# Kernel optimization log

Hardware: AMD Instinct MI355X
Metric: run time of the kernel (lower is better)

The kernel has to match this reference:

```python
import jax, jax.numpy as jnp
import numpy as np

K_POOL = 5

def _conv_lookahead(x, W):
    # Faithful to F.conv2d(pad=(fs//2+1,0)) followed by keeping the last L rows:
    # for fs=3 this reduces to out[t] = sum_j x[t+j] @ W[:,j,:].T (2 trailing zeros).
    # x: [..., L, E], W: [nf, fs, E] -> out [..., L, nf]
    fs = W.shape[1]
    L = x.shape[-2]
    pad = [(0, 0)] * (x.ndim - 2) + [(0, fs - 1), (0, 0)]
    xp = jnp.pad(x, pad)
    out = sum(jnp.einsum('...le,fe->...lf', jax.lax.dynamic_slice_in_dim(xp, j, L, axis=-2), W[:, j, :]) for j in range(fs))
    return out

def _cosine(q, s):
    # q: [B,Q,D], s: [B,S,L,D] -> [B,S,Q,L]
    num = jnp.einsum('bqd,bsld->bsql', q, s)
    qn = jnp.linalg.norm(q, axis=-1)  # [B,Q]
    sn = jnp.linalg.norm(s, axis=-1)  # [B,S,L]
    return num / (qn[:, None, :, None] * sn[:, :, None, :])

def _pool(sim, k=K_POOL):
    # sort-based k-max pooling over last dim -> (max, mean-of-top-k), matching torch.sort + slice
    top = jax.lax.top_k(sim, k)[0]            # [..., Q, k] descending
    return jnp.stack([top[..., 0], top.mean(-1)], axis=-1)  # [..., Q, 2]

def _bce(p, t):
    return -(t * jnp.log(p) + (1.0 - t) * jnp.log(1.0 - p)).mean()

def setup_inputs() -> dict:
    key = jax.random.key(0)
    ks = jax.random.split(key, 9)
    B, S, L, Q, V, E, NF, FS = 16, 48, 64, 32, 50000, 300, 256, 3
    return {
        'sentences': jax.random.randint(ks[0], (B, S, L), 0, V, dtype=jnp.int64 if jax.config.jax_enable_x64 else jnp.int32).astype(jnp.int32),
        'question': jax.random.randint(ks[1], (B, Q), 0, V).astype(jnp.int32),
        'target_sents': jax.random.randint(ks[2], (B, S), 0, 2).astype(jnp.int32),
        'target_docs': jax.random.randint(ks[3], (B,), 0, 2).astype(jnp.int32),
        'similarity_one_hot': jax.random.uniform(ks[4], (B, S, Q, L), dtype=jnp.float32),
        'embeds': jax.random.normal(ks[5], (V, E), dtype=jnp.float32),
        'conv_w': jax.random.normal(ks[6], (NF, FS, E), dtype=jnp.float32),
        'lin_w': jax.random.normal(ks[7], (1, 6), dtype=jnp.float32),
        'lin_b': jax.random.normal(ks[8], (1,), dtype=jnp.float32),
    }

def reference(sentences, question, target_sents, target_docs, similarity_one_hot, embeds, conv_w, lin_w, lin_b):
    q_emb = embeds[question]            # [B,Q,E]
    s_emb = embeds[sentences]           # [B,S,L,E]
    q_conv = _conv_lookahead(q_emb, conv_w)   # [B,Q,NF]
    s_conv = _conv_lookahead(s_emb, conv_w)   # [B,S,L,NF]

    sim_ins = _cosine(q_emb, s_emb)     # [B,S,Q,L]
    qmask = (question > 1).astype(sim_ins.dtype)   # [B,Q]
    smask = (sentences > 1).astype(sim_ins.dtype)  # [B,S,L]
    sim_ins = sim_ins * qmask[:, None, :, None] * smask[:, :, None, :]

    sim_sens = _cosine(q_conv, s_conv)  # [B,S,Q,L]

    feats = jnp.concatenate([_pool(sim_ins), _pool(sim_sens), _pool(similarity_one_hot)], axis=-1)  # [B,S,Q,6]
    lo = jax.nn.sigmoid(jnp.einsum('bsqf,of->bsqo', feats, lin_w)[..., 0] + lin_b[0])  # [B,S,Q]
    sent_output = lo.mean(-1)           # [B,S]

    sal = _bce(sent_output, target_sents.astype(sent_output.dtype))
    doc_emit = sent_output.max(-1)      # [B]
    dal = _bce(doc_emit, target_docs.astype(doc_emit.dtype))
    total_loss = (sal + dal) / 2.0
    return (total_loss, sent_output, doc_emit)
```

## Files before the change

kernel.cpp:

```cpp
#include <hip/hip_runtime.h>
#include <math.h>

#define NB 16
#define NS 48
#define NL 64
#define NQ 32
#define NE 300
#define NF 256
#define KP 320
#define QROWS 36

typedef __attribute__((ext_vector_type(8))) short short8;
typedef __attribute__((ext_vector_type(4))) float f32x4;

#define MFMA(a,b,c) __builtin_amdgcn_mfma_f32_16x16x32_bf16((a),(b),(c),0,0,0)

__device__ __forceinline__ unsigned short f2bf(float f) {
    unsigned u = __float_as_uint(f);
    u += 0x7fff + ((u >> 16) & 1);
    return (unsigned short)(u >> 16);
}

#define SE_PITCH 640
#define SC_PITCH 512
#define SIM_OFF (66 * 640)
#define SIM_PITCH 66
#define DYN_LDS (SIM_OFF + NQ * SIM_PITCH * 4)

__device__ __forceinline__ float wave_reduce_sum(float v) {
#pragma unroll
    for (int off = 32; off; off >>= 1) v += __shfl_xor(v, off, 64);
    return v;
}

__device__ __forceinline__ void top5_pool4(float v0, float v1, float v2, float v3,
                                           int lane, float* mx, float* mn) {
    float s0 = 0.f, s1 = 0.f, s2 = 0.f, s3 = 0.f;
    float x0 = 0.f, x1 = 0.f, x2 = 0.f, x3 = 0.f;
#pragma unroll
    for (int i = 0; i < 5; ++i) {
        float m0 = v0, m1 = v1, m2 = v2, m3 = v3;
#pragma unroll
        for (int off = 32; off; off >>= 1) {
            m0 = fmaxf(m0, __shfl_xor(m0, off, 64));
            m1 = fmaxf(m1, __shfl_xor(m1, off, 64));
            m2 = fmaxf(m2, __shfl_xor(m2, off, 64));
            m3 = fmaxf(m3, __shfl_xor(m3, off, 64));
        }
        if (i == 0) { x0 = m0; x1 = m1; x2 = m2; x3 = m3; }
        s0 += m0; s1 += m1; s2 += m2; s3 += m3;
        unsigned long long k0 = __ballot(v0 == m0);
        unsigned long long k1 = __ballot(v1 == m1);
        unsigned long long k2 = __ballot(v2 == m2);
        unsigned long long k3 = __ballot(v3 == m3);
        if (lane == __ffsll(k0) - 1) v0 = -3.4e38f;
        if (lane == __ffsll(k1) - 1) v1 = -3.4e38f;
        if (lane == __ffsll(k2) - 1) v2 = -3.4e38f;
        if (lane == __ffsll(k3) - 1) v3 = -3.4e38f;
    }
    mx[0] = x0; mx[1] = x1; mx[2] = x2; mx[3] = x3;
    mn[0] = s0 * 0.2f; mn[1] = s1 * 0.2f; mn[2] = s2 * 0.2f; mn[3] = s3 * 0.2f;
}

__global__ void wb2_kernel(const float* __restrict__ conv_w, short8* __restrict__ Wb2,
                           unsigned int* __restrict__ done_ctr) {
    if (blockIdx.x == 0 && threadIdx.x == 0) done_ctr[0] = 0u;
    int i = blockIdx.x * 256 + threadIdx.x;
    if (i >= 120 * 256) return;
    int rl = i & 15;
    int ftile = (i >> 4) & 15;
    int c = i >> 8;
    int kg = c & 3, rest = c >> 2;
    int ks = rest % 10, j = rest / 10;
    int f = ftile * 16 + rl;
    int k0 = ks * 32 + kg * 8;
    const float* src = conv_w + (size_t)(f * 3 + j) * NE;
    short8 h;
#pragma unroll
    for (int e = 0; e < 8; ++e) {
        int k = k0 + e;
        h[e] = (short)((k < NE) ? f2bf(src[k]) : (unsigned short)0);
    }
    Wb2[i] = h;
}

__global__ void qe_kernel(const int* __restrict__ question, const float* __restrict__ embeds,
                          unsigned short* __restrict__ qe, short8* __restrict__ qef,
                          float* __restrict__ q_norm) {
    int row = blockIdx.x;
    int b = row / QROWS, r = row % QROWS;
    int l = threadIdx.x;
    unsigned short* dst = qe + (size_t)row * KP;
    if (r < NQ) {
        int tok = question[b * NQ + r];
        const float4* rp = (const float4*)(embeds + (size_t)tok * NE);
        short8 h = {0, 0, 0, 0, 0, 0, 0, 0};
        float ss = 0.f;
        if (l < 38) {
            float4 v0 = rp[2 * l];
            ss += v0.x * v0.x + v0.y * v0.y + v0.z * v0.z + v0.w * v0.w;
            h[0] = (short)f2bf(v0.x); h[1] = (short)f2bf(v0.y);
            h[2] = (short)f2bf(v0.z); h[3] = (short)f2bf(v0.w);
            if (2 * l + 1 < 75) {
                float4 v1 = rp[2 * l + 1];
                ss += v1.x * v1.x + v1.y * v1.y + v1.z * v1.z + v1.w * v1.w;
                h[4] = (short)f2bf(v1.x); h[5] = (short)f2bf(v1.y);
                h[6] = (short)f2bf(v1.z); h[7] = (short)f2bf(v1.w);
            }
        }
        if (l < 40) {
            *(short8*)(dst + 8 * l) = h;
            qef[((size_t)(b * 2 + (r >> 4)) * 40 + l) * 16 + (r & 15)] = h;
        }
        ss = wave_reduce_sum(ss);
        if (l == 0) q_norm[b * NQ + r] = sqrtf(ss);
    } else {
        if (l < 40) {
            short8 z = {0, 0, 0, 0, 0, 0, 0, 0};
            *(short8*)(dst + 8 * l) = z;
        }
    }
}

__global__ __launch_bounds__(256) void qconv_mfma_kernel(
        const unsigned short* __restrict__ qe, const short8* __restrict__ Wb2,
        short8* __restrict__ qcf) {
    __shared__ unsigned short tile[NQ][72];
    int b = blockIdx.x >> 2, fq = blockIdx.x & 3;
    int tid = threadIdx.x, lane = tid & 63, w = tid >> 6;
    int rl = lane & 15, kg = lane >> 4;
    int ftile = fq * 4 + w;
    f32x4 acc0 = (f32x4){0.f, 0.f, 0.f, 0.f};
    f32x4 acc1 = (f32x4){0.f, 0.f, 0.f, 0.f};
    for (int j = 0; j < 3; ++j) {
#pragma unroll 2
        for (int ks = 0; ks < 10; ++ks) {
            int k = ks * 32 + kg * 8;
            int c = (j * 10 + ks) * 4 + kg;
            short8 a0 = *(const short8*)(qe + ((size_t)(b * QROWS) + rl + j) * KP + k);
            short8 a1 = *(const short8*)(qe + ((size_t)(b * QROWS) + 16 + rl + j) * KP + k);
            short8 bb = Wb2[(c * 16 + ftile) * 16 + rl];
            acc0 = MFMA(a0, bb, acc0);
            acc1 = MFMA(a1, bb, acc1);
        }
    }
    int fl = w * 16 + rl;
#pragma unroll
    for (int reg = 0; reg < 4; ++reg) {
        tile[kg * 4 + reg][fl] = f2bf(acc0[reg]);
        tile[16 + kg * 4 + reg][fl] = f2bf(acc1[reg]);
    }
    __syncthreads();
    int mh = tid >> 7, c_local = (tid >> 4) & 7, rl2 = tid & 15;
    short8 h = *(const short8*)(&tile[mh * 16 + rl2][c_local * 8]);
    qcf[((size_t)(b * 2 + mh) * 32 + 8 * fq + c_local) * 16 + rl2] = h;
}

__global__ __launch_bounds__(256) void qcn_kernel(const short8* __restrict__ qcf,
                                                  float* __restrict__ qc_norm) {
    __shared__ float part[2][16][8];
    int b = blockIdx.x;
    int tid = threadIdx.x;
    int mh = tid >> 7, sub = (tid >> 4) & 7, rl = tid & 15;
    const short8* base = qcf + ((size_t)(b * 2 + mh) * 32) * 16;
    float ss = 0.f;
#pragma unroll
    for (int i = 0; i < 4; ++i) {
        short8 h = base[(sub * 4 + i) * 16 + rl];
#pragma unroll
        for (int e = 0; e < 8; ++e) {
            float v = __uint_as_float(((unsigned)(unsigned short)h[e]) << 16);
            ss += v * v;
        }
    }
    part[mh][rl][sub] = ss;
    __syncthreads();
    if (tid < 32) {
        int m2 = tid >> 4, r2 = tid & 15;
        float s = 0.f;
#pragma unroll
        for (int k = 0; k < 8; ++k) s += part[m2][r2][k];
        qc_norm[b * NQ + m2 * 16 + r2] = sqrtf(s);
    }
}

extern __shared__ char ldsc[];
__global__ __launch_bounds__(256, 3) void fused6_kernel(
    const int* __restrict__ sentences, const int* __restrict__ question,
    const float* __restrict__ sim_oh, const float* __restrict__ embeds,
    const short8* __restrict__ Wb2,
    const short8* __restrict__ qef, const short8* __restrict__ qcf,
    const float* __restrict__ q_norm, const float* __restrict__ qc_norm,
    const float* __restrict__ lin_w, const float* __restrict__ lin_b,
    const int* __restrict__ tsent, const int* __restrict__ tdoc,
    unsigned int* __restrict__ done_ctr,
    float* __restrict__ sent_ws, float* __restrict__ d_out)
{
    __shared__ int toks[NL];
    __shared__ float smaskf[NL], snorm[NL], scnorm[NL];
    __shared__ float qn_s[NQ], qcn_s[NQ], qmf_s[NQ];
    __shared__ float wq[4];
    __shared__ float fpool[NQ][2];
    __shared__ int lastflag;
    __shared__ float red2[4];
    __shared__ float dred[NB];

    int tid = threadIdx.x, lane = tid & 63, w = tid >> 6;
    int rl = lane & 15, kg = lane >> 4;
    int bs = blockIdx.x, b = bs / NS;
    int t = (w << 4) + rl, t7 = t & 7;

    if (tid < NL) {
        int tk = sentences[(size_t)bs * NL + tid];
        toks[tid] = tk;
        smaskf[tid] = (tk > 1) ? 1.f : 0.f;
    } else if (tid < NL + NQ) {
        int q = tid - NL;
        qn_s[q] = q_norm[b * NQ + q];
    } else if (tid < NL + 2 * NQ) {
        int q = tid - NL - NQ;
        qcn_s[q] = qc_norm[b * NQ + q];
    } else if (tid < NL + 3 * NQ) {
        int q = tid - NL - 2 * NQ;
        qmf_s[q] = (question[b * NQ + q] > 1) ? 1.f : 0.f;
    }
    __syncthreads();

#pragma unroll 2
    for (int r = w; r < 66; r += 4) {
        char* rowbase = ldsc + r * SE_PITCH;
        int m7 = r & 7;
        if (r < NL) {
            const float4* rp = (const float4*)(embeds + (size_t)toks[r] * NE);
            {
                float4 v = rp[lane];
                ushort4 h = {f2bf(v.x), f2bf(v.y), f2bf(v.z), f2bf(v.w)};
                *(ushort4*)(rowbase + (((lane >> 1) ^ m7) << 4) + ((lane & 1) << 3)) = h;
            }
            if (lane < 11) {
                float4 v = rp[64 + lane];
                ushort4 h = {f2bf(v.x), f2bf(v.y), f2bf(v.z), f2bf(v.w)};
                int g = 64 + lane;
                *(ushort4*)(rowbase + (((g >> 1) ^ m7) << 4) + ((g & 1) << 3)) = h;
            }
            if (lane < 5) {
                int pk = 37 + ((lane + 1) >> 1);
                int sub = ((lane + 1) & 1) << 3;
                *(unsigned long long*)(rowbase + ((pk ^ m7) << 4) + sub) = 0ull;
            }
        } else {
            if (lane < 40) {
                uint4 z = {0, 0, 0, 0};
                *(uint4*)(rowbase + (lane << 4)) = z;
            }
        }
    }
    __syncthreads();

    {
        f32x4 iacc0 = (f32x4){0.f, 0.f, 0.f, 0.f};
        f32x4 iacc1 = (f32x4){0.f, 0.f, 0.f, 0.f};
        f32x4 nB = (f32x4){0.f, 0.f, 0.f, 0.f};
        const short8* qf = qef + (size_t)(b * 80) * 16;
#pragma unroll 2
        for (int ks = 0; ks < 10; ++ks) {
            int c = ks * 4 + kg;
            short8 bB = *(const short8*)(ldsc + t * SE_PITCH + ((c ^ t7) << 4));
            short8 a0 = qf[c * 16 + rl];
            short8 a1 = qf[(40 + c) * 16 + rl];
            iacc0 = MFMA(a0, bB, iacc0);
            iacc1 = MFMA(a1, bB, iacc1);
            nB = MFMA(bB, bB, nB);
        }
        if (kg == (rl >> 2)) snorm[t] = sqrtf(nB[rl & 3]);
        __syncthreads();

        float inv_t = smaskf[t] / snorm[t];
#pragma unroll
        for (int reg = 0; reg < 4; ++reg) {
            int q0 = kg * 4 + reg;
            float s0 = iacc0[reg] / qn_s[q0] * inv_t * qmf_s[q0];
            *(float*)(ldsc + SIM_OFF + (q0 * SIM_PITCH + t) * 4) = s0;
            int q1 = 16 + kg * 4 + reg;
            float s1 = iacc1[reg] / qn_s[q1] * inv_t * qmf_s[q1];
            *(float*)(ldsc + SIM_OFF + (q1 * SIM_PITCH + t) * 4) = s1;
        }
    }
    __syncthreads();

    {
        int q0 = w << 3;
        float v[8];
#pragma unroll
        for (int qi = 0; qi < 8; ++qi)
            v[qi] = *(float*)(ldsc + SIM_OFF + ((q0 + qi) * SIM_PITCH + lane) * 4);
        float mx[4], mn[4];
        top5_pool4(v[0], v[1], v[2], v[3], lane, mx, mn);
        if (lane == 0)
#pragma unroll
            for (int p = 0; p < 4; ++p) { fpool[q0 + p][0] = mx[p]; fpool[q0 + p][1] = mn[p]; }
        top5_pool4(v[4], v[5], v[6], v[7], lane, mx, mn);
        if (lane == 0)
#pragma unroll
            for (int p = 0; p < 4; ++p) { fpool[q0 + 4 + p][0] = mx[p]; fpool[q0 + 4 + p][1] = mn[p]; }
    }

    f32x4 cacc[4][4];
#pragma unroll
    for (int m = 0; m < 4; ++m)
#pragma unroll
        for (int nn = 0; nn < 4; ++nn) cacc[m][nn] = (f32x4){0.f, 0.f, 0.f, 0.f};
    for (int j = 0; j < 3; ++j) {
#pragma unroll 2
        for (int ks = 0; ks < 10; ++ks) {
            int c = (j * 10 + ks) * 4 + kg;
            short8 a[4], bb[4];
#pragma unroll
            for (int m = 0; m < 4; ++m) {
                int row = m * 16 + rl + j;
                a[m] = *(const short8*)(ldsc + row * SE_PITCH +
                                        ((((ks << 2) + kg) ^ (row & 7)) << 4));
            }
#pragma unroll
            for (int nn = 0; nn < 4; ++nn)
                bb[nn] = Wb2[(c * 16 + (w * 4 + nn)) * 16 + rl];
#pragma unroll
            for (int m = 0; m < 4; ++m)
#pragma unroll
                for (int nn = 0; nn < 4; ++nn)
                    cacc[m][nn] = MFMA(a[m], bb[nn], cacc[m][nn]);
        }
    }
    __syncthreads();

#pragma unroll
    for (int m = 0; m < 4; ++m)
#pragma unroll
        for (int nn = 0; nn < 4; ++nn) {
            int f = (w * 4 + nn) * 16 + rl;
#pragma unroll
            for (int reg = 0; reg < 4; ++reg) {
                int tr = m * 16 + kg * 4 + reg;
                *(unsigned short*)(ldsc + tr * SC_PITCH +
                                   (((f >> 3) ^ (tr & 7)) << 4) + ((f & 7) << 1)) =
                    f2bf(cacc[m][nn][reg]);
            }
        }
    __syncthreads();

    float oh[8];
#pragma unroll
    for (int qi = 0; qi < 8; ++qi) {
        int q = (w << 3) + qi;
        oh[qi] = sim_oh[((size_t)bs * NQ + q) * NL + lane];
    }
    {
        f32x4 sacc0 = (f32x4){0.f, 0.f, 0.f, 0.f};
        f32x4 sacc1 = (f32x4){0.f, 0.f, 0.f, 0.f};
        f32x4 nB = (f32x4){0.f, 0.f, 0.f, 0.f};
        const short8* qc = qcf + (size_t)(b * 64) * 16;
#pragma unroll 2
        for (int ks = 0; ks < 8; ++ks) {
            int c = ks * 4 + kg;
            short8 bB = *(const short8*)(ldsc + t * SC_PITCH + ((c ^ t7) << 4));
            short8 a0 = qc[c * 16 + rl];
            short8 a1 = qc[(32 + c) * 16 + rl];
            sacc0 = MFMA(a0, bB, sacc0);
            sacc1 = MFMA(a1, bB, sacc1);
            nB = MFMA(bB, bB, nB);
        }
        if (kg == (rl >> 2)) scnorm[t] = sqrtf(nB[rl & 3]);
        __syncthreads();

        float inv_t = 1.f / scnorm[t];
#pragma unroll
        for (int reg = 0; reg < 4; ++reg) {
            int q0 = kg * 4 + reg;
            *(float*)(ldsc + SIM_OFF + (q0 * SIM_PITCH + t) * 4) =
                sacc0[reg] / qcn_s[q0] * inv_t;
            int q1 = 16 + kg * 4 + reg;
            *(float*)(ldsc + SIM_OFF + (q1 * SIM_PITCH + t) * 4) =
                sacc1[reg] / qcn_s[q1] * inv_t;
        }
    }
    __syncthreads();

    {
        float lw0 = lin_w[0], lw1 = lin_w[1], lw2 = lin_w[2];
        float lw3 = lin_w[3], lw4 = lin_w[4], lw5 = lin_w[5];
        float lb = lin_b[0];
        int q0 = w << 3;
        float sv[8];
#pragma unroll
        for (int qi = 0; qi < 8; ++qi)
            sv[qi] = *(float*)(ldsc + SIM_OFF + ((q0 + qi) * SIM_PITCH + lane) * 4);
        float mxs[8], mns[8], mxo[8], mno[8];
        top5_pool4(sv[0], sv[1], sv[2], sv[3], lane, mxs, mns);
        top5_pool4(sv[4], sv[5], sv[6], sv[7], lane, mxs + 4, mns + 4);
        top5_pool4(oh[0], oh[1], oh[2], oh[3], lane, mxo, mno);
        top5_pool4(oh[4], oh[5], oh[6], oh[7], lane, mxo + 4, mno + 4);
        float psum = 0.f;
#pragma unroll
        for (int qi = 0; qi < 8; ++qi) {
            float f0 = fpool[q0 + qi][0], f1 = fpool[q0 + qi][1];
            float z = f0 * lw0 + f1 * lw1 + mxs[qi] * lw2 + mns[qi] * lw3 +
                      mxo[qi] * lw4 + mno[qi] * lw5 + lb;
            psum += 1.f / (1.f + expf(-z));
        }
        if (lane == 0) wq[w] = psum;
    }
    __syncthreads();
    if (tid == 0) {
        float sent = (wq[0] + wq[1] + wq[2] + wq[3]) * (1.f / 32.f);
        __hip_atomic_store(&sent_ws[bs], sent, __ATOMIC_RELEASE, __HIP_MEMORY_SCOPE_AGENT);
        d_out[1 + bs] = sent;
        unsigned old = atomicAdd(done_ctr, 1u);
        lastflag = (old == (unsigned)(NB * NS - 1)) ? 1 : 0;
    }
    __syncthreads();

    if (lastflag) {
        float acc_l = 0.f;
        for (int i = tid; i < NB * NS; i += 256) {
            float p = __hip_atomic_load(&sent_ws[i], __ATOMIC_ACQUIRE, __HIP_MEMORY_SCOPE_AGENT);
            float tt2 = (float)tsent[i];
            acc_l += tt2 * logf(p) + (1.f - tt2) * logf(1.f - p);
        }
        acc_l = wave_reduce_sum(acc_l);
        if ((tid & 63) == 0) red2[tid >> 6] = acc_l;
        if (tid < NB) {
            float m = -3.4e38f;
            for (int s = 0; s < NS; ++s)
                m = fmaxf(m, __hip_atomic_load(&sent_ws[tid * NS + s], __ATOMIC_ACQUIRE,
                                               __HIP_MEMORY_SCOPE_AGENT));
            d_out[1 + NB * NS + tid] = m;
            float tt2 = (float)tdoc[tid];
            dred[tid] = tt2 * logf(m) + (1.f - tt2) * logf(1.f - m);
        }
        __syncthreads();
        if (tid == 0) {
            float sal = -(red2[0] + red2[1] + red2[2] + red2[3]) / (float)(NB * NS);
            float dsum = 0.f;
            for (int i = 0; i < NB; ++i) dsum += dred[i];
            float dal = -dsum / (float)NB;
            d_out[0] = 0.5f * (sal + dal);
        }
    }
}

extern "C" void kernel_launch(void* const* d_in, const int* in_sizes, int n_in,
                              void* d_out, int out_size, void* d_ws, size_t ws_size,
                              hipStream_t stream) {
    const int* sentences = (const int*)d_in[0];
    const int* question = (const int*)d_in[1];
    const int* tsent = (const int*)d_in[2];
    const int* tdoc = (const int*)d_in[3];
    const float* sim_oh = (const float*)d_in[4];
    const float* embeds = (const float*)d_in[5];
    const float* conv_w = (const float*)d_in[6];
    const float* lin_w = (const float*)d_in[7];
    const float* lin_b = (const float*)d_in[8];
    float* out = (float*)d_out;

    char* wsc = (char*)d_ws;
    short8* Wb2            = (short8*)(wsc);
    unsigned short* qe_old = (unsigned short*)(wsc + 491520);
    short8* qef            = (short8*)(wsc + 860160);
    short8* qcf            = (short8*)(wsc + 1187840);
    float* q_norm          = (float*)(wsc + 1449984);
    float* qc_norm         = (float*)(wsc + 1452032);
    float* sent_ws         = (float*)(wsc + 1454080);
    unsigned int* done_ctr = (unsigned int*)(wsc + 1457152);

    hipFuncSetAttribute(reinterpret_cast<const void*>(fused6_kernel),
                        hipFuncAttributeMaxDynamicSharedMemorySize, DYN_LDS);

    wb2_kernel<<<120, 256, 0, stream>>>(conv_w, Wb2, done_ctr);
    qe_kernel<<<NB * QROWS, 64, 0, stream>>>(question, embeds, qe_old, qef, q_norm);
    qconv_mfma_kernel<<<NB * 4, 256, 0, stream>>>(qe_old, Wb2, qcf);
    qcn_kernel<<<NB, 256, 0, stream>>>(qcf, qc_norm);
    fused6_kernel<<<NB * NS, 256, DYN_LDS, stream>>>(
        sentences, question, sim_oh, embeds, Wb2, qef, qcf, q_norm, qc_norm,
        lin_w, lin_b, tsent, tdoc, done_ctr, sent_ws, out);
}
```

Baseline: 130.6 us.

## Double fused kernel block to 512 threads, splitting work across eight waves

Raises the fused per-sentence kernel from 4 to 8 waves per block. Each wave now handles half the question rows in the cosine MFMAs and half the filter tiles in the conv GEMM, which halves per-wave accumulator registers. The goal is more waves in flight per block to hide the embedding gather and global loads, and less serial work per wave. The cost is redundant B-operand LDS reads across waves (the norm MFMA is kept only on waves 0-3) and larger blocks. Occupancy now depends on LDS size and the new launch bounds.

After: 173.4 us. +32.7%, slower.

```diff
diff --git a/kernel.cpp b/kernel.cpp
--- a/kernel.cpp
+++ b/kernel.cpp
@@ -185,7 +185,7 @@
 }
 
 extern __shared__ char ldsc[];
-__global__ __launch_bounds__(256, 3) void fused6_kernel(
+__global__ __launch_bounds__(512, 4) void fused7_kernel(
     const int* __restrict__ sentences, const int* __restrict__ question,
     const float* __restrict__ sim_oh, const float* __restrict__ embeds,
     const short8* __restrict__ Wb2,
@@ -199,16 +199,17 @@
     __shared__ int toks[NL];
     __shared__ float smaskf[NL], snorm[NL], scnorm[NL];
     __shared__ float qn_s[NQ], qcn_s[NQ], qmf_s[NQ];
-    __shared__ float wq[4];
+    __shared__ float wq[8];
     __shared__ float fpool[NQ][2];
     __shared__ int lastflag;
-    __shared__ float red2[4];
+    __shared__ float red2[8];
     __shared__ float dred[NB];
 
     int tid = threadIdx.x, lane = tid & 63, w = tid >> 6;
     int rl = lane & 15, kg = lane >> 4;
+    int mh = w >> 2, tt = w & 3;
     int bs = blockIdx.x, b = bs / NS;
-    int t = (w << 4) + rl, t7 = t & 7;
+    int t = (tt << 4) + rl, t7 = t & 7;
 
     if (tid < NL) {
         int tk = sentences[(size_t)bs * NL + tid];
@@ -227,7 +228,7 @@
     __syncthreads();
 
 #pragma unroll 2
-    for (int r = w; r < 66; r += 4) {
+    for (int r = w; r < 66; r += 8) {
         char* rowbase = ldsc + r * SE_PITCH;
         int m7 = r & 7;
         if (r < NL) {
@@ -258,63 +259,53 @@
     __syncthreads();
 
     {
-        f32x4 iacc0 = (f32x4){0.f, 0.f, 0.f, 0.f};
-        f32x4 iacc1 = (f32x4){0.f, 0.f, 0.f, 0.f};
+        f32x4 iacc = (f32x4){0.f, 0.f, 0.f, 0.f};
         f32x4 nB = (f32x4){0.f, 0.f, 0.f, 0.f};
-        const short8* qf = qef + (size_t)(b * 80) * 16;
+        const short8* qf = qef + ((size_t)(b * 2 + mh) * 40) * 16;
 #pragma unroll 2
         for (int ks = 0; ks < 10; ++ks) {
             int c = ks * 4 + kg;
             short8 bB = *(const short8*)(ldsc + t * SE_PITCH + ((c ^ t7) << 4));
             short8 a0 = qf[c * 16 + rl];
-            short8 a1 = qf[(40 + c) * 16 + rl];
-            iacc0 = MFMA(a0, bB, iacc0);
-            iacc1 = MFMA(a1, bB, iacc1);
-            nB = MFMA(bB, bB, nB);
-        }
-        if (kg == (rl >> 2)) snorm[t] = sqrtf(nB[rl & 3]);
+            iacc = MFMA(a0, bB, iacc);
+            if (w < 4) nB = MFMA(bB, bB, nB);
+        }
+        if (w < 4 && kg == (rl >> 2)) snorm[t] = sqrtf(nB[rl & 3]);
         __syncthreads();
 
         float inv_t = smaskf[t] / snorm[t];
 #pragma unroll
         for (int reg = 0; reg < 4; ++reg) {
-            int q0 = kg * 4 + reg;
-            float s0 = iacc0[reg] / qn_s[q0] * inv_t * qmf_s[q0];
-            *(float*)(ldsc + SIM_OFF + (q0 * SIM_PITCH + t) * 4) = s0;
-            int q1 = 16 + kg * 4 + reg;
-            float s1 = iacc1[reg] / qn_s[q1] * inv_t * qmf_s[q1];
-            *(float*)(ldsc + SIM_OFF + (q1 * SIM_PITCH + t) * 4) = s1;
+            int q = mh * 16 + kg * 4 + reg;
+            float s0 = iacc[reg] / qn_s[q] * inv_t * qmf_s[q];
+            *(float*)(ldsc + SIM_OFF + (q * SIM_PITCH + t) * 4) = s0;
         }
     }
     __syncthreads();
 
     {
-        int q0 = w << 3;
-        float v[8];
-#pragma unroll
-        for (int qi = 0; qi < 8; ++qi)
-            v[qi] = *(float*)(ldsc + SIM_OFF + ((q0 + qi) * SIM_PITCH + lane) * 4);
+        int q0 = w << 2;
+        float v0 = *(float*)(ldsc + SIM_OFF + ((q0 + 0) * SIM_PITCH + lane) * 4);
+        float v1 = *(float*)(ldsc + SIM_OFF + ((q0 + 1) * SIM_PITCH + lane) * 4);
+        float v2 = *(float*)(ldsc + SIM_OFF + ((q0 + 2) * SIM_PITCH + lane) * 4);
+        float v3 = *(float*)(ldsc + SIM_OFF + ((q0 + 3) * SIM_PITCH + lane) * 4);
         float mx[4], mn[4];
-        top5_pool4(v[0], v[1], v[2], v[3], lane, mx, mn);
+        top5_pool4(v0, v1, v2, v3, lane, mx, mn);
         if (lane == 0)
 #pragma unroll
             for (int p = 0; p < 4; ++p) { fpool[q0 + p][0] = mx[p]; fpool[q0 + p][1] = mn[p]; }
-        top5_pool4(v[4], v[5], v[6], v[7], lane, mx, mn);
-        if (lane == 0)
-#pragma unroll
-            for (int p = 0; p < 4; ++p) { fpool[q0 + 4 + p][0] = mx[p]; fpool[q0 + 4 + p][1] = mn[p]; }
-    }
-
-    f32x4 cacc[4][4];
+    }
+
+    f32x4 cacc[4][2];
 #pragma unroll
     for (int m = 0; m < 4; ++m)
 #pragma unroll
-        for (int nn = 0; nn < 4; ++nn) cacc[m][nn] = (f32x4){0.f, 0.f, 0.f, 0.f};
+        for (int nn = 0; nn < 2; ++nn) cacc[m][nn] = (f32x4){0.f, 0.f, 0.f, 0.f};
     for (int j = 0; j < 3; ++j) {
 #pragma unroll 2
         for (int ks = 0; ks < 10; ++ks) {
             int c = (j * 10 + ks) * 4 + kg;
-            short8 a[4], bb[4];
+            short8 a[4], bb[2];
 #pragma unroll
             for (int m = 0; m < 4; ++m) {
                 int row = m * 16 + rl + j;
@@ -322,12 +313,12 @@
                                         ((((ks << 2) + kg) ^ (row & 7)) << 4));
             }
 #pragma unroll
-            for (int nn = 0; nn < 4; ++nn)
-                bb[nn] = Wb2[(c * 16 + (w * 4 + nn)) * 16 + rl];
+            for (int nn = 0; nn < 2; ++nn)
+                bb[nn] = Wb2[(c * 16 + ((w << 1) + nn)) * 16 + rl];
 #pragma unroll
             for (int m = 0; m < 4; ++m)
 #pragma unroll
-                for (int nn = 0; nn < 4; ++nn)
+                for (int nn = 0; nn < 2; ++nn)
                     cacc[m][nn] = MFMA(a[m], bb[nn], cacc[m][nn]);
         }
     }
@@ -336,8 +327,8 @@
 #pragma unroll
     for (int m = 0; m < 4; ++m)
 #pragma unroll
-        for (int nn = 0; nn < 4; ++nn) {
-            int f = (w * 4 + nn) * 16 + rl;
+        for (int nn = 0; nn < 2; ++nn) {
+            int f = ((w << 1) + nn) * 16 + rl;
 #pragma unroll
             for (int reg = 0; reg < 4; ++reg) {
                 int tr = m * 16 + kg * 4 + reg;
@@ -348,39 +339,33 @@
         }
     __syncthreads();
 
-    float oh[8];
-#pragma unroll
-    for (int qi = 0; qi < 8; ++qi) {
-        int q = (w << 3) + qi;
+    float oh[4];
+#pragma unroll
+    for (int qi = 0; qi < 4; ++qi) {
+        int q = (w << 2) + qi;
         oh[qi] = sim_oh[((size_t)bs * NQ + q) * NL + lane];
     }
     {
-        f32x4 sacc0 = (f32x4){0.f, 0.f, 0.f, 0.f};
-        f32x4 sacc1 = (f32x4){0.f, 0.f, 0.f, 0.f};
+        f32x4 sacc = (f32x4){0.f, 0.f, 0.f, 0.f};
         f32x4 nB = (f32x4){0.f, 0.f, 0.f, 0.f};
-        const short8* qc = qcf + (size_t)(b * 64) * 16;
+        const short8* qc = qcf + ((size_t)(b * 2 + mh) * 32) * 16;
 #pragma unroll 2
         for (int ks = 0; ks < 8; ++ks) {
             int c = ks * 4 + kg;
             short8 bB = *(const short8*)(ldsc + t * SC_PITCH + ((c ^ t7) << 4));
             short8 a0 = qc[c * 16 + rl];
-            short8 a1 = qc[(32 + c) * 16 + rl];
-            sacc0 = MFMA(a0, bB, sacc0);
-            sacc1 = MFMA(a1, bB, sacc1);
-            nB = MFMA(bB, bB, nB);
-        }
-        if (kg == (rl >> 2)) scnorm[t] = sqrtf(nB[rl & 3]);
+            sacc = MFMA(a0, bB, sacc);
+            if (w < 4) nB = MFMA(bB, bB, nB);
+        }
+        if (w < 4 && kg == (rl >> 2)) scnorm[t] = sqrtf(nB[rl & 3]);
         __syncthreads();
 
         float inv_t = 1.f / scnorm[t];
 #pragma unroll
         for (int reg = 0; reg < 4; ++reg) {
-            int q0 = kg * 4 + reg;
-            *(float*)(ldsc + SIM_OFF + (q0 * SIM_PITCH + t) * 4) =
-                sacc0[reg] / qcn_s[q0] * inv_t;
-            int q1 = 16 + kg * 4 + reg;
-            *(float*)(ldsc + SIM_OFF + (q1 * SIM_PITCH + t) * 4) =
-                sacc1[reg] / qcn_s[q1] * inv_t;
+            int q = mh * 16 + kg * 4 + reg;
+            *(float*)(ldsc + SIM_OFF + (q * SIM_PITCH + t) * 4) =
+                sacc[reg] / qcn_s[q] * inv_t;
         }
     }
     __syncthreads();
@@ -389,19 +374,17 @@
         float lw0 = lin_w[0], lw1 = lin_w[1], lw2 = lin_w[2];
         float lw3 = lin_w[3], lw4 = lin_w[4], lw5 = lin_w[5];
         float lb = lin_b[0];
-        int q0 = w << 3;
-        float sv[8];
-#pragma unroll
-        for (int qi = 0; qi < 8; ++qi)
-            sv[qi] = *(float*)(ldsc + SIM_OFF + ((q0 + qi) * SIM_PITCH + lane) * 4);
-        float mxs[8], mns[8], mxo[8], mno[8];
-        top5_pool4(sv[0], sv[1], sv[2], sv[3], lane, mxs, mns);
-        top5_pool4(sv[4], sv[5], sv[6], sv[7], lane, mxs + 4, mns + 4);
+        int q0 = w << 2;
+        float sv0 = *(float*)(ldsc + SIM_OFF + ((q0 + 0) * SIM_PITCH + lane) * 4);
+        float sv1 = *(float*)(ldsc + SIM_OFF + ((q0 + 1) * SIM_PITCH + lane) * 4);
+        float sv2 = *(float*)(ldsc + SIM_OFF + ((q0 + 2) * SIM_PITCH + lane) * 4);
+        float sv3 = *(float*)(ldsc + SIM_OFF + ((q0 + 3) * SIM_PITCH + lane) * 4);
+        float mxs[4], mns[4], mxo[4], mno[4];
+        top5_pool4(sv0, sv1, sv2, sv3, lane, mxs, mns);
         top5_pool4(oh[0], oh[1], oh[2], oh[3], lane, mxo, mno);
-        top5_pool4(oh[4], oh[5], oh[6], oh[7], lane, mxo + 4, mno + 4);
         float psum = 0.f;
 #pragma unroll
-        for (int qi = 0; qi < 8; ++qi) {
+        for (int qi = 0; qi < 4; ++qi) {
             float f0 = fpool[q0 + qi][0], f1 = fpool[q0 + qi][1];
             float z = f0 * lw0 + f1 * lw1 + mxs[qi] * lw2 + mns[qi] * lw3 +
                       mxo[qi] * lw4 + mno[qi] * lw5 + lb;
@@ -411,7 +394,8 @@
     }
     __syncthreads();
     if (tid == 0) {
-        float sent = (wq[0] + wq[1] + wq[2] + wq[3]) * (1.f / 32.f);
+        float sent = (wq[0] + wq[1] + wq[2] + wq[3] + wq[4] + wq[5] + wq[6] + wq[7])
+                     * (1.f / 32.f);
         __hip_atomic_store(&sent_ws[bs], sent, __ATOMIC_RELEASE, __HIP_MEMORY_SCOPE_AGENT);
         d_out[1 + bs] = sent;
         unsigned old = atomicAdd(done_ctr, 1u);
@@ -421,7 +405,7 @@
 
     if (lastflag) {
         float acc_l = 0.f;
-        for (int i = tid; i < NB * NS; i += 256) {
+        for (int i = tid; i < NB * NS; i += 512) {
             float p = __hip_atomic_load(&sent_ws[i], __ATOMIC_ACQUIRE, __HIP_MEMORY_SCOPE_AGENT);
             float tt2 = (float)tsent[i];
             acc_l += tt2 * logf(p) + (1.f - tt2) * logf(1.f - p);
@@ -439,7 +423,8 @@
         }
         __syncthreads();
         if (tid == 0) {
-            float sal = -(red2[0] + red2[1] + red2[2] + red2[3]) / (float)(NB * NS);
+            float sal = -(red2[0] + red2[1] + red2[2] + red2[3] +
+                          red2[4] + red2[5] + red2[6] + red2[7]) / (float)(NB * NS);
             float dsum = 0.f;
             for (int i = 0; i < NB; ++i) dsum += dred[i];
             float dal = -dsum / (float)NB;
@@ -472,14 +457,14 @@
     float* sent_ws         = (float*)(wsc + 1454080);
     unsigned int* done_ctr = (unsigned int*)(wsc + 1457152);
 
-    hipFuncSetAttribute(reinterpret_cast<const void*>(fused6_kernel),
+    hipFuncSetAttribute(reinterpret_cast<const void*>(fused7_kernel),
                         hipFuncAttributeMaxDynamicSharedMemorySize, DYN_LDS);
 
     wb2_kernel<<<120, 256, 0, stream>>>(conv_w, Wb2, done_ctr);
     qe_kernel<<<NB * QROWS, 64, 0, stream>>>(question, embeds, qe_old, qef, q_norm);
     qconv_mfma_kernel<<<NB * 4, 256, 0, stream>>>(qe_old, Wb2, qcf);
     qcn_kernel<<<NB, 256, 0, stream>>>(qcf, qc_norm);
-    fused6_kernel<<<NB * NS, 256, DYN_LDS, stream>>>(
+    fused7_kernel<<<NB * NS, 512, DYN_LDS, stream>>>(
         sentences, question, sim_oh, embeds, Wb2, qef, qcf, q_norm, qc_norm,
         lin_w, lin_b, tsent, tdoc, done_ctr, sent_ws, out);
 }
```

## Split fused kernel into pack, word-similarity, and conv-similarity kernels

Applied to the files above, without the earlier changes.

The monolithic per-sentence kernel is split into three launches. A pack kernel gathers embeddings, converts them to bf16 in an MFMA-friendly global layout and computes row norms in fp32. A separate kernel computes word-level cosine top-k pooling. The conv kernel then reads its A operands directly from global memory instead of LDS, which shrinks LDS use and drops the occupancy hint. This is meant to raise occupancy and shorten the serial prologue, at the cost of extra launches and global round-trips for the packed embeddings and pooled features.

Result: slower. 151.5 us (+16.0%).

```diff
diff --git a/kernel.cpp b/kernel.cpp
--- a/kernel.cpp
+++ b/kernel.cpp
@@ -20,12 +20,6 @@
     u += 0x7fff + ((u >> 16) & 1);
     return (unsigned short)(u >> 16);
 }
-
-#define SE_PITCH 640
-#define SC_PITCH 512
-#define SIM_OFF (66 * 640)
-#define SIM_PITCH 66
-#define DYN_LDS (SIM_OFF + NQ * SIM_PITCH * 4)
 
 __device__ __forceinline__ float wave_reduce_sum(float v) {
 #pragma unroll
@@ -184,23 +178,125 @@
     }
 }
 
+__global__ __launch_bounds__(256) void pack_kernel(
+        const int* __restrict__ sentences, const float* __restrict__ embeds,
+        short8* __restrict__ sB, float* __restrict__ snorm_g) {
+    __shared__ unsigned short stg[16][328];
+    __shared__ int toks[NL];
+    int bs = blockIdx.x;
+    int tid = threadIdx.x, lane = tid & 63, w = tid >> 6;
+    if (tid < NL) toks[tid] = sentences[(size_t)bs * NL + tid];
+    __syncthreads();
+    short8* sbb = sB + (size_t)bs * 40 * 64;
+    for (int it = 0; it < 4; ++it) {
+#pragma unroll
+        for (int i = 0; i < 4; ++i) {
+            int r16 = w * 4 + i;
+            int r = it * 16 + r16;
+            const float4* rp = (const float4*)(embeds + (size_t)toks[r] * NE);
+            float ss;
+            {
+                float4 v = rp[lane];
+                ss = v.x * v.x + v.y * v.y + v.z * v.z + v.w * v.w;
+                ushort4 h = {f2bf(v.x), f2bf(v.y), f2bf(v.z), f2bf(v.w)};
+                *(ushort4*)&stg[r16][4 * lane] = h;
+            }
+            if (lane < 11) {
+                float4 v = rp[64 + lane];
+                ss += v.x * v.x + v.y * v.y + v.z * v.z + v.w * v.w;
+                ushort4 h = {f2bf(v.x), f2bf(v.y), f2bf(v.z), f2bf(v.w)};
+                *(ushort4*)&stg[r16][256 + 4 * lane] = h;
+            } else if (lane < 16) {
+                ushort4 z = {0, 0, 0, 0};
+                *(ushort4*)&stg[r16][256 + 4 * lane] = z;
+            }
+            ss = wave_reduce_sum(ss);
+            if (lane == 0) snorm_g[bs * NL + r] = sqrtf(ss);
+        }
+        __syncthreads();
+        {
+            int c = tid >> 4, rl = tid & 15;
+            for (; c < 40; c += 16) {
+                short8 h = *(const short8*)&stg[rl][c * 8];
+                sbb[(size_t)c * 64 + it * 16 + rl] = h;
+            }
+        }
+        __syncthreads();
+    }
+}
+
+__global__ __launch_bounds__(256) void ins_kernel(
+        const int* __restrict__ sentences, const int* __restrict__ question,
+        const short8* __restrict__ sB, const short8* __restrict__ qef,
+        const float* __restrict__ snorm_g, const float* __restrict__ q_norm,
+        float2* __restrict__ fpool_ins) {
+    __shared__ float sim[NQ][66];
+    __shared__ float qn_s[NQ], qmf_s[NQ];
+    int bs = blockIdx.x, b = bs / NS;
+    int tid = threadIdx.x, lane = tid & 63, w = tid >> 6;
+    int rl = lane & 15, kg = lane >> 4;
+    int t = (w << 4) + rl;
+    if (tid < NQ) qn_s[tid] = q_norm[b * NQ + tid];
+    else if (tid < 2 * NQ) {
+        int q = tid - NQ;
+        qmf_s[q] = (question[b * NQ + q] > 1) ? 1.f : 0.f;
+    }
+    float sn_t = snorm_g[bs * NL + t];
+    float sm_t = (sentences[(size_t)bs * NL + t] > 1) ? 1.f : 0.f;
+    __syncthreads();
+    f32x4 i0 = (f32x4){0.f, 0.f, 0.f, 0.f};
+    f32x4 i1 = (f32x4){0.f, 0.f, 0.f, 0.f};
+    const short8* qf = qef + (size_t)(b * 80) * 16;
+    const short8* sbb = sB + (size_t)bs * 40 * 64;
+#pragma unroll 2
+    for (int ks = 0; ks < 10; ++ks) {
+        int c = ks * 4 + kg;
+        short8 bB = sbb[(size_t)c * 64 + t];
+        i0 = MFMA(qf[c * 16 + rl], bB, i0);
+        i1 = MFMA(qf[(40 + c) * 16 + rl], bB, i1);
+    }
+    float inv_t = sm_t / sn_t;
+#pragma unroll
+    for (int reg = 0; reg < 4; ++reg) {
+        int q0 = kg * 4 + reg;
+        sim[q0][t] = i0[reg] / qn_s[q0] * inv_t * qmf_s[q0];
+        int q1 = 16 + kg * 4 + reg;
+        sim[q1][t] = i1[reg] / qn_s[q1] * inv_t * qmf_s[q1];
+    }
+    __syncthreads();
+    int q0 = w << 3;
+    float mx[4], mn[4];
+    top5_pool4(sim[q0 + 0][lane], sim[q0 + 1][lane], sim[q0 + 2][lane], sim[q0 + 3][lane],
+               lane, mx, mn);
+    if (lane == 0)
+#pragma unroll
+        for (int p = 0; p < 4; ++p)
+            fpool_ins[(size_t)bs * NQ + q0 + p] = (float2){mx[p], mn[p]};
+    top5_pool4(sim[q0 + 4][lane], sim[q0 + 5][lane], sim[q0 + 6][lane], sim[q0 + 7][lane],
+               lane, mx, mn);
+    if (lane == 0)
+#pragma unroll
+        for (int p = 0; p < 4; ++p)
+            fpool_ins[(size_t)bs * NQ + q0 + 4 + p] = (float2){mx[p], mn[p]};
+}
+
+#define SC_PITCH 512
+#define SIM_OFF (64 * SC_PITCH)
+#define SIM_PITCH 66
+#define DYN_LDS (SIM_OFF + NQ * SIM_PITCH * 4)
 extern __shared__ char ldsc[];
-__global__ __launch_bounds__(256, 3) void fused6_kernel(
-    const int* __restrict__ sentences, const int* __restrict__ question,
-    const float* __restrict__ sim_oh, const float* __restrict__ embeds,
-    const short8* __restrict__ Wb2,
-    const short8* __restrict__ qef, const short8* __restrict__ qcf,
-    const float* __restrict__ q_norm, const float* __restrict__ qc_norm,
-    const float* __restrict__ lin_w, const float* __restrict__ lin_b,
-    const int* __restrict__ tsent, const int* __restrict__ tdoc,
-    unsigned int* __restrict__ done_ctr,
-    float* __restrict__ sent_ws, float* __restrict__ d_out)
-{
-    __shared__ int toks[NL];
-    __shared__ float smaskf[NL], snorm[NL], scnorm[NL];
-    __shared__ float qn_s[NQ], qcn_s[NQ], qmf_s[NQ];
+__global__ __launch_bounds__(256) void convsens_kernel(
+        const int* __restrict__ question, const float* __restrict__ sim_oh,
+        const short8* __restrict__ sB, const short8* __restrict__ Wb2,
+        const short8* __restrict__ qcf, const float* __restrict__ qc_norm,
+        const float2* __restrict__ fpool_ins,
+        const float* __restrict__ lin_w, const float* __restrict__ lin_b,
+        const int* __restrict__ tsent, const int* __restrict__ tdoc,
+        unsigned int* __restrict__ done_ctr,
+        float* __restrict__ sent_ws, float* __restrict__ d_out) {
+    __shared__ float scnorm[NL];
+    __shared__ float qcn_s[NQ];
     __shared__ float wq[4];
-    __shared__ float fpool[NQ][2];
     __shared__ int lastflag;
     __shared__ float red2[4];
     __shared__ float dred[NB];
@@ -210,101 +306,9 @@
     int bs = blockIdx.x, b = bs / NS;
     int t = (w << 4) + rl, t7 = t & 7;
 
-    if (tid < NL) {
-        int tk = sentences[(size_t)bs * NL + tid];
-        toks[tid] = tk;
-        smaskf[tid] = (tk > 1) ? 1.f : 0.f;
-    } else if (tid < NL + NQ) {
-        int q = tid - NL;
-        qn_s[q] = q_norm[b * NQ + q];
-    } else if (tid < NL + 2 * NQ) {
-        int q = tid - NL - NQ;
-        qcn_s[q] = qc_norm[b * NQ + q];
-    } else if (tid < NL + 3 * NQ) {
-        int q = tid - NL - 2 * NQ;
-        qmf_s[q] = (question[b * NQ + q] > 1) ? 1.f : 0.f;
-    }
-    __syncthreads();
-
-#pragma unroll 2
-    for (int r = w; r < 66; r += 4) {
-        char* rowbase = ldsc + r * SE_PITCH;
-        int m7 = r & 7;
-        if (r < NL) {
-            const float4* rp = (const float4*)(embeds + (size_t)toks[r] * NE);
-            {
-                float4 v = rp[lane];
-                ushort4 h = {f2bf(v.x), f2bf(v.y), f2bf(v.z), f2bf(v.w)};
-                *(ushort4*)(rowbase + (((lane >> 1) ^ m7) << 4) + ((lane & 1) << 3)) = h;
-            }
-            if (lane < 11) {
-                float4 v = rp[64 + lane];
-                ushort4 h = {f2bf(v.x), f2bf(v.y), f2bf(v.z), f2bf(v.w)};
-                int g = 64 + lane;
-                *(ushort4*)(rowbase + (((g >> 1) ^ m7) << 4) + ((g & 1) << 3)) = h;
-            }
-            if (lane < 5) {
-                int pk = 37 + ((lane + 1) >> 1);
-                int sub = ((lane + 1) & 1) << 3;
-                *(unsigned long long*)(rowbase + ((pk ^ m7) << 4) + sub) = 0ull;
-            }
-        } else {
-            if (lane < 40) {
-                uint4 z = {0, 0, 0, 0};
-                *(uint4*)(rowbase + (lane << 4)) = z;
-            }
-        }
-    }
-    __syncthreads();
-
-    {
-        f32x4 iacc0 = (f32x4){0.f, 0.f, 0.f, 0.f};
-        f32x4 iacc1 = (f32x4){0.f, 0.f, 0.f, 0.f};
-        f32x4 nB = (f32x4){0.f, 0.f, 0.f, 0.f};
-        const short8* qf = qef + (size_t)(b * 80) * 16;
-#pragma unroll 2
-        for (int ks = 0; ks < 10; ++ks) {
-            int c = ks * 4 + kg;
-            short8 bB = *(const short8*)(ldsc + t * SE_PITCH + ((c ^ t7) << 4));
-            short8 a0 = qf[c * 16 + rl];
-            short8 a1 = qf[(40 + c) * 16 + rl];
-            iacc0 = MFMA(a0, bB, iacc0);
-            iacc1 = MFMA(a1, bB, iacc1);
-            nB = MFMA(bB, bB, nB);
-        }
-        if (kg == (rl >> 2)) snorm[t] = sqrtf(nB[rl & 3]);
-        __syncthreads();
-
-        float inv_t = smaskf[t] / snorm[t];
-#pragma unroll
-        for (int reg = 0; reg < 4; ++reg) {
-            int q0 = kg * 4 + reg;
-            float s0 = iacc0[reg] / qn_s[q0] * inv_t * qmf_s[q0];
-            *(float*)(ldsc + SIM_OFF + (q0 * SIM_PITCH + t) * 4) = s0;
-            int q1 = 16 + kg * 4 + reg;
-            float s1 = iacc1[reg] / qn_s[q1] * inv_t * qmf_s[q1];
-            *(float*)(ldsc + SIM_OFF + (q1 * SIM_PITCH + t) * 4) = s1;
-        }
-    }
-    __syncthreads();
-
-    {
-        int q0 = w << 3;
-        float v[8];
-#pragma unroll
-        for (int qi = 0; qi < 8; ++qi)
-            v[qi] = *(float*)(ldsc + SIM_OFF + ((q0 + qi) * SIM_PITCH + lane) * 4);
-        float mx[4], mn[4];
-        top5_pool4(v[0], v[1], v[2], v[3], lane, mx, mn);
-        if (lane == 0)
-#pragma unroll
-            for (int p = 0; p < 4; ++p) { fpool[q0 + p][0] = mx[p]; fpool[q0 + p][1] = mn[p]; }
-        top5_pool4(v[4], v[5], v[6], v[7], lane, mx, mn);
-        if (lane == 0)
-#pragma unroll
-            for (int p = 0; p < 4; ++p) { fpool[q0 + 4 + p][0] = mx[p]; fpool[q0 + 4 + p][1] = mn[p]; }
-    }
-
+    if (tid < NQ) qcn_s[tid] = qc_norm[b * NQ + tid];
+
+    const short8* sbb = sB + (size_t)bs * 40 * 64;
     f32x4 cacc[4][4];
 #pragma unroll
     for (int m = 0; m < 4; ++m)
@@ -313,13 +317,16 @@
     for (int j = 0; j < 3; ++j) {
 #pragma unroll 2
         for (int ks = 0; ks < 10; ++ks) {
+            int cA = ks * 4 + kg;
             int c = (j * 10 + ks) * 4 + kg;
             short8 a[4], bb[4];
 #pragma unroll
-            for (int m = 0; m < 4; ++m) {
-                int row = m * 16 + rl + j;
-                a[m] = *(const short8*)(ldsc + row * SE_PITCH +
-                                        ((((ks << 2) + kg) ^ (row & 7)) << 4));
+            for (int m = 0; m < 3; ++m)
+                a[m] = sbb[(size_t)cA * 64 + m * 16 + rl + j];
+            {
+                int row3 = 48 + rl + j;
+                short8 z = {0, 0, 0, 0, 0, 0, 0, 0};
+                a[3] = (row3 < 64) ? sbb[(size_t)cA * 64 + row3] : z;
             }
 #pragma unroll
             for (int nn = 0; nn < 4; ++nn)
@@ -363,10 +370,8 @@
         for (int ks = 0; ks < 8; ++ks) {
             int c = ks * 4 + kg;
             short8 bB = *(const short8*)(ldsc + t * SC_PITCH + ((c ^ t7) << 4));
-            short8 a0 = qc[c * 16 + rl];
-            short8 a1 = qc[(32 + c) * 16 + rl];
-            sacc0 = MFMA(a0, bB, sacc0);
-            sacc1 = MFMA(a1, bB, sacc1);
+            sacc0 = MFMA(qc[c * 16 + rl], bB, sacc0);
+            sacc1 = MFMA(qc[(32 + c) * 16 + rl], bB, sacc1);
             nB = MFMA(bB, bB, nB);
         }
         if (kg == (rl >> 2)) scnorm[t] = sqrtf(nB[rl & 3]);
@@ -402,8 +407,8 @@
         float psum = 0.f;
 #pragma unroll
         for (int qi = 0; qi < 8; ++qi) {
-            float f0 = fpool[q0 + qi][0], f1 = fpool[q0 + qi][1];
-            float z = f0 * lw0 + f1 * lw1 + mxs[qi] * lw2 + mns[qi] * lw3 +
+            float2 fp = fpool_ins[(size_t)bs * NQ + q0 + qi];
+            float z = fp.x * lw0 + fp.y * lw1 + mxs[qi] * lw2 + mns[qi] * lw3 +
                       mxo[qi] * lw4 + mno[qi] * lw5 + lb;
             psum += 1.f / (1.f + expf(-z));
         }
@@ -471,15 +476,21 @@
     float* qc_norm         = (float*)(wsc + 1452032);
     float* sent_ws         = (float*)(wsc + 1454080);
     unsigned int* done_ctr = (unsigned int*)(wsc + 1457152);
-
-    hipFuncSetAttribute(reinterpret_cast<const void*>(fused6_kernel),
+    float* snorm_g         = (float*)(wsc + 1457168);
+    float2* fpool_ins      = (float2*)(wsc + 1653776);
+    short8* sB             = (short8*)(wsc + 1850384);
+
+    hipFuncSetAttribute(reinterpret_cast<const void*>(convsens_kernel),
                         hipFuncAttributeMaxDynamicSharedMemorySize, DYN_LDS);
 
     wb2_kernel<<<120, 256, 0, stream>>>(conv_w, Wb2, done_ctr);
     qe_kernel<<<NB * QROWS, 64, 0, stream>>>(question, embeds, qe_old, qef, q_norm);
     qconv_mfma_kernel<<<NB * 4, 256, 0, stream>>>(qe_old, Wb2, qcf);
     qcn_kernel<<<NB, 256, 0, stream>>>(qcf, qc_norm);
-    fused6_kernel<<<NB * NS, 256, DYN_LDS, stream>>>(
-        sentences, question, sim_oh, embeds, Wb2, qef, qcf, q_norm, qc_norm,
+    pack_kernel<<<NB * NS, 256, 0, stream>>>(sentences, embeds, sB, snorm_g);
+    ins_kernel<<<NB * NS, 256, 0, stream>>>(sentences, question, sB, qef,
+                                            snorm_g, q_norm, fpool_ins);
+    convsens_kernel<<<NB * NS, 256, DYN_LDS, stream>>>(
+        question, sim_oh, sB, Wb2, qcf, qc_norm, fpool_ins,
         lin_w, lin_b, tsent, tdoc, done_ctr, sent_ws, out);
 }
```
